# Optimization experiments

Measured on AMD Instinct MI355X. Metric: run time of the kernel, lower is better.

## Reference

```python
import jax, jax.numpy as jnp
import numpy as np

PRE_NMS_TOP_K = 6000   # 'test' mode
POST_NMS_TOP_K = 300   # 'test' mode
IOU_THRESHOLD = 0.7


def setup_inputs() -> dict:
    key = jax.random.key(0)
    k1, k2, k3, k4 = jax.random.split(key, 4)
    B, A, H, W = 1, 9, 64, 96
    N = H * W * A  # 55296 anchors
    pred_cls = jax.random.normal(k1, (B, 2 * A, H, W), dtype=jnp.float32)
    pred_loc = jax.random.normal(k2, (B, 4 * A, H, W), dtype=jnp.float32) * 0.1
    # anchors in normalized (cx, cy, w, h) format
    cxcy = jax.random.uniform(k3, (N, 2), dtype=jnp.float32)
    wh = jax.random.uniform(k4, (N, 2), dtype=jnp.float32) * 0.2 + 0.02
    anchor = jnp.concatenate([cxcy, wh], axis=-1)
    return {"pred_cls": pred_cls, "pred_loc": pred_loc, "anchor": anchor}


def _decode_to_xy(loc, anchor):
    # decode: t(cx,cy) * a(w,h) + a(cx,cy); exp(t(w,h)) * a(w,h); then cxcy -> xyxy
    cxcy = loc[:, :2] * anchor[:, 2:] + anchor[:, :2]
    wh = jnp.exp(loc[:, 2:]) * anchor[:, 2:]
    return jnp.concatenate([cxcy - wh * 0.5, cxcy + wh * 0.5], axis=-1)


def _iou_matrix(boxes):
    # boxes: [N,4] xyxy -> [N,N] IoU
    area = (boxes[:, 2] - boxes[:, 0]) * (boxes[:, 3] - boxes[:, 1])
    lt = jnp.maximum(boxes[:, None, :2], boxes[None, :, :2])  # [N,N,2]
    rb = jnp.minimum(boxes[:, None, 2:], boxes[None, :, 2:])  # [N,N,2]
    wh = jnp.clip(rb - lt, 0.0)
    inter = wh[..., 0] * wh[..., 1]
    union = area[:, None] + area[None, :] - inter
    return inter / jnp.maximum(union, 1e-12)


def _nms_keep(boxes, iou_threshold):
    # boxes already sorted by descending score -> greedy NMS
    n = boxes.shape[0]
    iou = _iou_matrix(boxes)
    idx = jnp.arange(n)

    def body(i, keep):
        suppress = (iou[i] > iou_threshold) & (idx > i)
        return jnp.where(keep[i], keep & ~suppress, keep)

    return jax.lax.fori_loop(0, n, body, jnp.ones((n,), dtype=bool))


def reference(pred_cls, pred_loc, anchor):
    B = pred_cls.shape[0]
    # NCHW -> NHWC -> [N, 2] / [N, 4]  (batch squeezed, B == 1)
    cls = jnp.transpose(pred_cls, (0, 2, 3, 1)).reshape(B, -1, 2)[0]
    loc = jnp.transpose(pred_loc, (0, 2, 3, 1)).reshape(B, -1, 4)[0]

    roi = jnp.clip(_decode_to_xy(loc, anchor), 0.0, 1.0)           # [N,4]
    scores = jax.nn.sigmoid(cls)[:, 1]                              # [N]

    order = jnp.argsort(-scores)[:PRE_NMS_TOP_K]                    # descending
    roi = roi[order]                                                # [K,4]

    keep = _nms_keep(roi, IOU_THRESHOLD)                            # [K] bool
    # kept boxes first (stable -> preserves score order), take top 300
    sel = jnp.argsort(jnp.where(keep, 0, 1), stable=True)[:POST_NMS_TOP_K]
    valid = keep[sel]
    # pad with zeros if fewer than 300 boxes survive NMS (torch returns a
    # dynamically-sized tensor; we keep a fixed [300,4] with zero padding)
    return jnp.where(valid[:, None], roi[sel], 0.0)
```

## Files before the change

### kernel.cpp

```cpp
#include <hip/hip_runtime.h>


#define ADIM 9
#define NANCH 55296
#define HWSZ 6144
#define CH_U4 1536
#define TOT_U4 13824
#define SAMP_U4 3456
#define TOPK 6000
#define OUTK 300
#define NBINS 16384
#define CAP 8192
#define SCAP 1024
#define SRANK 128
#define MROWS 512
#define MW 8
#define THR 0.7f

typedef unsigned long long u64;
typedef unsigned int u32;

__device__ __forceinline__ u32 flipu(u32 b) {
    u32 u = (b & 0x80000000u) ? ~b : (b | 0x80000000u);
    return ~u;
}

__device__ __forceinline__ bool iou_gt(float4 a, float aa, float4 b, float ba) {
    float ix = fminf(a.z, b.z) - fmaxf(a.x, b.x);
    float iy = fminf(a.w, b.w) - fmaxf(a.y, b.y);
    float inter = fmaxf(ix, 0.f) * fmaxf(iy, 0.f);
    float u = fmaxf(aa + ba - inter, 1e-12f);
    float d = __builtin_fmaf(-THR, u, inter);
    if (__builtin_fabsf(d) > 1e-6f * u) return d > 0.f;
    return inter / u > THR;
}

__device__ __forceinline__ float4 decode_box(const float* __restrict__ loc,
                                             const float* __restrict__ anc, u32 n) {
    u32 a = n % 9u, hw = n / 9u;
    float t0 = loc[(4 * a + 0) * HWSZ + hw];
    float t1 = loc[(4 * a + 1) * HWSZ + hw];
    float t2 = loc[(4 * a + 2) * HWSZ + hw];
    float t3 = loc[(4 * a + 3) * HWSZ + hw];
    float4 an = reinterpret_cast<const float4*>(anc)[n];
    float cx = t0 * an.z + an.x;
    float cy = t1 * an.w + an.y;
    float bw = expf(t2) * an.z;
    float bh = expf(t3) * an.w;
    return make_float4(fminf(fmaxf(cx - bw * 0.5f, 0.f), 1.f),
                       fminf(fmaxf(cy - bh * 0.5f, 0.f), 1.f),
                       fminf(fmaxf(cx + bw * 0.5f, 0.f), 1.f),
                       fminf(fmaxf(cy + bh * 0.5f, 0.f), 1.f));
}

__device__ __forceinline__ u64 sx64(u64 v, int m) {
    u32 lo = __shfl_xor((u32)(v & 0xffffffffu), m, 64);
    u32 hi = __shfl_xor((u32)(v >> 32), m, 64);
    return ((u64)hi << 32) | lo;
}

__device__ __forceinline__ u64 ce64(u64 v, int j, int lane, bool up) {
    u64 pv = sx64(v, j);
    u64 mn = (pv < v) ? pv : v;
    u64 mx = (pv < v) ? v : pv;
    return (((lane & j) == 0) == up) ? mn : mx;
}

__device__ __forceinline__ uint4 ld_cls4(const uint4* __restrict__ cls4, int i) {
    int ch = i / CH_U4;
    int e4 = i - ch * CH_U4;
    return cls4[(2 * ch + 1) * CH_U4 + e4];
}

__device__ __forceinline__ u32 block_scan(u32 s, int wid, int lane, u32* wsum) {
    u32 x = s;
    #pragma unroll
    for (int d = 1; d < 64; d <<= 1) {
        u32 y = __shfl_up(x, (unsigned)d, 64);
        if (lane >= d) x += y;
    }
    if (lane == 63) wsum[wid] = x;
    __syncthreads();
    if (wid == 0) {
        u32 w = (lane < 16) ? wsum[lane] : 0u;
        #pragma unroll
        for (int d = 1; d < 16; d <<= 1) {
            u32 y = __shfl_up(w, (unsigned)d, 64);
            if (lane >= d) w += y;
        }
        if (lane < 16) wsum[lane] = w;
    }
    __syncthreads();
    return x + (wid ? wsum[wid - 1] : 0u);
}

__device__ __forceinline__ u32 find_cutoff(const u32* hist, u32 thresh, int tid,
                                           int wid, int lane, u32* wsum, u32* sB) {
    u32 h[16];
    const uint4* h4 = reinterpret_cast<const uint4*>(hist);
    #pragma unroll
    for (int k = 0; k < 4; ++k) {
        uint4 v = h4[tid * 4 + k];
        h[4 * k + 0] = v.x; h[4 * k + 1] = v.y; h[4 * k + 2] = v.z; h[4 * k + 3] = v.w;
    }
    u32 s = 0;
    #pragma unroll
    for (int b = 0; b < 16; ++b) s += h[b];
    u32 incl = block_scan(s, wid, lane, wsum);
    u32 before = incl - s;
    if (before < thresh && incl >= thresh) {
        u32 run = before;
        #pragma unroll
        for (int b = 0; b < 16; ++b) {
            run += h[b];
            if (run >= thresh) { sB[0] = (u32)(tid * 16 + b); break; }
        }
    }
    __syncthreads();
    u32 r = sB[0];
    __syncthreads();
    return r;
}

__global__ void __launch_bounds__(1024) k_scanrank(const float* __restrict__ cls,
                                                   const float* __restrict__ loc,
                                                   const float* __restrict__ anc,
                                                   u32* __restrict__ wsMeta,
                                                   float4* __restrict__ boxS,
                                                   float* __restrict__ areaS) {
    __shared__ u32 hist[NBINS];
    __shared__ __align__(16) u32 sfs[SCAP];
    __shared__ u32 sidx[SCAP];
    __shared__ u32 wsum[16];
    __shared__ u32 sB[2];
    __shared__ u32 shu[2];

    const int tid = threadIdx.x;
    const int wid = tid >> 6;
    const int lane = tid & 63;
    const uint4* cls4 = reinterpret_cast<const uint4*>(cls);

    u64* h64 = (u64*)hist;
    for (int i = tid; i < NBINS / 2; i += 1024) h64[i] = 0ull;
    if (tid < 2) shu[tid] = 0;
    __syncthreads();
    {
        uint4 s0 = ld_cls4(cls4, 4 * tid);
        uint4 s1 = ld_cls4(cls4, 4 * (tid + 1024));
        uint4 s2 = ld_cls4(cls4, 4 * (tid + 2048));
        bool has3 = tid < (SAMP_U4 - 3072);
        uint4 s3 = has3 ? ld_cls4(cls4, 4 * (tid + 3072)) : make_uint4(0u,0u,0u,0u);
        atomicAdd(&hist[flipu(s0.x) >> 18], 1u); atomicAdd(&hist[flipu(s0.y) >> 18], 1u);
        atomicAdd(&hist[flipu(s0.z) >> 18], 1u); atomicAdd(&hist[flipu(s0.w) >> 18], 1u);
        atomicAdd(&hist[flipu(s1.x) >> 18], 1u); atomicAdd(&hist[flipu(s1.y) >> 18], 1u);
        atomicAdd(&hist[flipu(s1.z) >> 18], 1u); atomicAdd(&hist[flipu(s1.w) >> 18], 1u);
        atomicAdd(&hist[flipu(s2.x) >> 18], 1u); atomicAdd(&hist[flipu(s2.y) >> 18], 1u);
        atomicAdd(&hist[flipu(s2.z) >> 18], 1u); atomicAdd(&hist[flipu(s2.w) >> 18], 1u);
        if (has3) {
            atomicAdd(&hist[flipu(s3.x) >> 18], 1u); atomicAdd(&hist[flipu(s3.y) >> 18], 1u);
            atomicAdd(&hist[flipu(s3.z) >> 18], 1u); atomicAdd(&hist[flipu(s3.w) >> 18], 1u);
        }
    }
    __syncthreads();
    const u32 B1 = find_cutoff(hist, SRANK, tid, wid, lane, wsum, sB);
    const u32 K1 = (B1 + 1u) << 18;

    u64 bm = 0;
    u32 cnt = 0;
    #pragma unroll
    for (int half = 0; half < 2; ++half) {
        uint4 buf[7];
        #pragma unroll
        for (int kk = 0; kk < 7; ++kk) {
            int i = (half * 7 + kk) * 1024 + tid;
            buf[kk] = (i < TOT_U4) ? ld_cls4(cls4, i) : make_uint4(0xFFFFFFFFu,0xFFFFFFFFu,0xFFFFFFFFu,0xFFFFFFFFu);
        }
        #pragma unroll
        for (int kk = 0; kk < 7; ++kk) {
            int i = (half * 7 + kk) * 1024 + tid;
            if (i < TOT_U4) {
                #pragma unroll
                for (int c = 0; c < 4; ++c) {
                    u32 b = (c == 0) ? buf[kk].x : (c == 1) ? buf[kk].y
                          : (c == 2) ? buf[kk].z : buf[kk].w;
                    if (flipu(b) < K1) {
                        cnt++;
                        bm |= 1ull << ((half * 7 + kk) * 4 + c);
                    }
                }
            }
        }
    }
    u32 incl = block_scan(cnt, wid, lane, wsum);
    u32 base = incl - cnt;
    if (tid == 1023) shu[0] = incl;
    __syncthreads();
    const u32 csRaw = shu[0];
    const u32 cs = csRaw < SCAP ? csRaw : SCAP;
    if (blockIdx.x == 0 && tid == 0) { wsMeta[0] = csRaw; wsMeta[1] = B1; }
    if (csRaw > SCAP) return;

    {
        u64 m = bm;
        u32 o = base;
        while (m) {
            int b = __ffsll((unsigned long long)m) - 1;
            m &= m - 1;
            int kk = b >> 2, c = b & 3;
            int i = kk * 1024 + tid;
            uint4 v = ld_cls4(cls4, i);
            u32 raw = (c == 0) ? v.x : (c == 1) ? v.y : (c == 2) ? v.z : v.w;
            int ch = i / CH_U4;
            int e4 = i - ch * CH_U4;
            u32 n = (u32)((e4 * 4 + c) * ADIM + ch);
            if (o < SCAP) { sfs[o] = flipu(raw); sidx[o] = n; }
            o++;
        }
    }
    if (tid >= (int)cs) { sfs[tid] = 0xFFFFFFFFu; sidx[tid] = 0xFFFFFFFFu; }
    __syncthreads();

    const int ci = blockIdx.x * 64 + (tid >> 4);
    const int p = tid & 15;
    const u32 myf = sfs[ci];
    const u32 myi = sidx[ci];
    u32 r = 0;
    #pragma unroll 8
    for (int k = 0; k < 64; ++k) {
        int j = k * 16 + p;
        u32 fj = sfs[j];
        u32 ij = sidx[j];
        r += (fj < myf) || (fj == myf && ij < myi);
    }
    r += __shfl_xor(r, 1, 64);
    r += __shfl_xor(r, 2, 64);
    r += __shfl_xor(r, 4, 64);
    r += __shfl_xor(r, 8, 64);
    if (p == 0 && (u32)ci < csRaw) {
        float4 b = decode_box(loc, anc, myi);
        boxS[r] = b;
        areaS[r] = (b.z - b.x) * (b.w - b.y);
    }
}

__global__ void __launch_bounds__(1024) k_mat(const u32* __restrict__ wsMeta,
                                              const float4* __restrict__ boxS,
                                              const float* __restrict__ areaS,
                                              u32* __restrict__ maskG32) {
    __shared__ float4 B[MROWS];
    __shared__ float  A[MROWS];
    __shared__ u32 M32[32][16];
    const int tid = threadIdx.x;
    const u32 csRaw = wsMeta[0];
    if (csRaw > SCAP) return;
    const u32 rowsv = csRaw < MROWS ? csRaw : MROWS;

    if (tid < MROWS) { B[tid] = boxS[tid]; A[tid] = areaS[tid]; }
    if (tid < 512) M32[tid >> 4][tid & 15] = 0u;
    __syncthreads();

    const int rl = tid >> 5;
    const int sub = tid & 31;
    const int row = blockIdx.x + 16 * rl;
    if (row < (int)rowsv) {
        const int j0 = sub * 16;
        int jmax = row < j0 + 16 ? row : j0 + 16;
        if (j0 < jmax) {
            float4 rb = B[row];
            float rba = A[row];
            u32 bits = 0;
            #pragma unroll 4
            for (int j = j0; j < jmax; ++j)
                if (iou_gt(rb, rba, B[j], A[j])) bits |= 1u << (j - j0);
            if (bits) atomicOr(&M32[rl][sub >> 1], bits << ((sub & 1) * 16));
        }
    }
    __syncthreads();
    if (tid < 512) {
        int rl2 = tid >> 4, w = tid & 15;
        int row2 = blockIdx.x + 16 * rl2;
        maskG32[row2 * 16 + w] = M32[rl2][w];
    }
}

__global__ void __launch_bounds__(1024) k_greedy(const float* __restrict__ cls,
                                                 const float* __restrict__ loc,
                                                 const float* __restrict__ anc,
                                                 const u32* __restrict__ wsMeta,
                                                 const float4* __restrict__ boxS,
                                                 const float* __restrict__ areaS,
                                                 const u32* __restrict__ maskG32,
                                                 float4* __restrict__ out) {
    __shared__ u64 cand[CAP];
    __shared__ u64 smask[MROWS][MW];
    __shared__ float4 sbox[SCAP];
    __shared__ float  sarea[SCAP];
    __shared__ float4 kept[OUTK];
    __shared__ float  karea[OUTK];
    __shared__ float4 cbox[64];
    __shared__ float  carea[64];
    __shared__ u64 supw[16];
    __shared__ u64 sbyp[1024];
    __shared__ u32 wsum[16];
    __shared__ u32 sB[2];
    __shared__ u32 shu[8];

    const int tid = threadIdx.x;
    const int wid = tid >> 6;
    const int lane = tid & 63;
    u32* hist = (u32*)cand;
    const uint4* cls4 = reinterpret_cast<const uint4*>(cls);

    const u32 csRaw = wsMeta[0];
    const u32 cs = csRaw < SCAP ? csRaw : SCAP;
    const bool fast = (csRaw <= SCAP);

    if (tid < 8) shu[tid] = 0;
    sbox[tid] = boxS[tid];
    sarea[tid] = areaS[tid];
    {
        u32* sm32 = (u32*)smask;
        #pragma unroll
        for (int k = 0; k < 8; ++k) sm32[k * 1024 + tid] = maskG32[k * 1024 + tid];
    }
    __syncthreads();

    if (fast) {
        const u32 rowsv = cs < MROWS ? cs : MROWS;
        if (wid == 0) {
            u32 kc = 0, nexti0 = 0;
            u64 K[MW];
            #pragma unroll
            for (int w = 0; w < MW; ++w) K[w] = 0ull;
            #pragma unroll
            for (int cw = 0; cw < MW; ++cw) {
                u32 i0 = (u32)cw * 64u;
                if (i0 < rowsv && kc < OUTK) {
                    u32 ci = i0 + (u32)lane;
                    bool valid = ci < rowsv;
                    u64 myw[MW];
                    #pragma unroll
                    for (int w = 0; w < MW; ++w) myw[w] = valid ? smask[ci][w] : 0ull;
                    u64 supk = 0;
                    #pragma unroll
                    for (int w = 0; w < MW; ++w) supk |= myw[w] & K[w];
                    bool ia = valid && (supk == 0ull);
                    u64 inch = myw[cw] & ((1ull << lane) - 1ull);
                    u64 A = __ballot(ia ? 1 : 0);
                    for (int itx = 0; itx < 64; ++itx) {
                        bool na = ia && ((inch & A) == 0ull);
                        u64 A2 = __ballot(na ? 1 : 0);
                        if (A2 == A) break;
                        A = A2;
                    }
                    bool kp = (A >> lane) & 1;
                    u32 rank = (u32)__popcll(A & ((1ull << lane) - 1ull));
                    if (kp && kc + rank < OUTK) {
                        float4 c = sbox[ci];
                        kept[kc + rank] = c;
                        karea[kc + rank] = sarea[ci];
                        out[kc + rank] = c;
                    }
                    K[cw] = A;
                    kc += (u32)__popcll(A);
                    nexti0 = i0 + 64;
                }
            }
            if (lane == 0) {
                shu[4] = kc > OUTK ? OUTK : kc;
                shu[5] = nexti0;
            }
        }

        const u32 limit = cs;
        while (true) {
            __syncthreads();
            u32 kc = shu[4], i0 = shu[5];
            if (kc >= OUTK || i0 >= limit) break;
            u32 ci = i0 + (u32)lane;
            bool valid = ci < limit;
            float4 c = sbox[valid ? ci : 0];
            float ca = sarea[valid ? ci : 0];

            bool sup = false;
            for (u32 j = (u32)wid; j < kc; j += 16)
                sup = sup || iou_gt(c, ca, kept[j], karea[j]);
            u64 bal = __ballot(sup ? 1 : 0);
            if (lane == 0) supw[wid] = bal;

            u64 sby = 0;
            u32 smax = 4u * wid + 4u; if (smax > 63u) smax = 63u;
            for (u32 s = 4u * wid + 1u; s <= smax; ++s) {
                u32 p = ((u32)lane + s) & 63u;
                if (p < (u32)lane && (i0 + p) < limit)
                    if (iou_gt(c, ca, sbox[i0 + p], sarea[i0 + p])) sby |= (1ull << p);
            }
            sbyp[wid * 64 + lane] = sby;
            __syncthreads();

            if (wid == 0) {
                u64 sup64 = 0, sbyfull = 0;
                #pragma unroll
                for (int w = 0; w < 16; ++w) { sup64 |= supw[w]; sbyfull |= sbyp[w * 64 + lane]; }
                bool ia = valid && !((sup64 >> lane) & 1);
                u64 A = __ballot(ia ? 1 : 0);
                for (int itx = 0; itx < 64; ++itx) {
                    bool na = ia && ((sbyfull & A) == 0);
                    u64 A2 = __ballot(na ? 1 : 0);
                    if (A2 == A) break;
                    A = A2;
                }
                bool kp = (A >> lane) & 1;
                u32 rank = (u32)__popcll(A & ((1ull << lane) - 1ull));
                if (kp && kc + rank < OUTK) {
                    kept[kc + rank] = c; karea[kc + rank] = ca; out[kc + rank] = c;
                }
                if (lane == 0) {
                    u32 nk = kc + (u32)__popcll(A);
                    shu[4] = nk > OUTK ? OUTK : nk;
                    shu[5] = i0 + 64;
                }
            }
        }
    }

    __syncthreads();
    if (shu[4] < OUTK) {
        const u32 consumed = fast ? cs : 0u;
        u64* h64 = (u64*)hist;
        for (int i = tid; i < NBINS / 2; i += 1024) h64[i] = 0ull;
        __syncthreads();
        #pragma unroll
        for (int half = 0; half < 2; ++half) {
            uint4 buf[7];
            #pragma unroll
            for (int kk = 0; kk < 7; ++kk) {
                int i = (half * 7 + kk) * 1024 + tid;
                buf[kk] = (i < TOT_U4) ? ld_cls4(cls4, i) : make_uint4(0u,0u,0u,0u);
            }
            #pragma unroll
            for (int kk = 0; kk < 7; ++kk) {
                int i = (half * 7 + kk) * 1024 + tid;
                if (i < TOT_U4) {
                    atomicAdd(&hist[flipu(buf[kk].x) >> 18], 1u);
                    atomicAdd(&hist[flipu(buf[kk].y) >> 18], 1u);
                    atomicAdd(&hist[flipu(buf[kk].z) >> 18], 1u);
                    atomicAdd(&hist[flipu(buf[kk].w) >> 18], 1u);
                }
            }
        }
        __syncthreads();
        const u32 B2 = find_cutoff(hist, TOPK, tid, wid, lane, wsum, sB);
        u64 bm2 = 0;
        u32 cnt2 = 0;
        #pragma unroll
        for (int half = 0; half < 2; ++half) {
            uint4 buf[7];
            #pragma unroll
            for (int kk = 0; kk < 7; ++kk) {
                int i = (half * 7 + kk) * 1024 + tid;
                buf[kk] = (i < TOT_U4) ? ld_cls4(cls4, i) : make_uint4(0xFFFFFFFFu,0xFFFFFFFFu,0xFFFFFFFFu,0xFFFFFFFFu);
            }
            #pragma unroll
            for (int kk = 0; kk < 7; ++kk) {
                int i = (half * 7 + kk) * 1024 + tid;
                if (i < TOT_U4) {
                    #pragma unroll
                    for (int c = 0; c < 4; ++c) {
                        u32 b = (c == 0) ? buf[kk].x : (c == 1) ? buf[kk].y
                              : (c == 2) ? buf[kk].z : buf[kk].w;
                        if ((flipu(b) >> 18) <= B2) {
                            cnt2++;
                            bm2 |= 1ull << ((half * 7 + kk) * 4 + c);
                        }
                    }
                }
            }
        }
        __syncthreads();
        for (int i = tid; i < CAP; i += 1024) cand[i] = ~0ull;
        u32 incl2 = block_scan(cnt2, wid, lane, wsum);
        u32 base2 = incl2 - cnt2;
        if (tid == 1023) shu[1] = incl2;
        __syncthreads();
        {
            u64 m2 = bm2;
            u32 o = base2;
            while (m2) {
                int b = __ffsll((unsigned long long)m2) - 1;
                m2 &= m2 - 1;
                int kk = b >> 2, c = b & 3;
                int i = kk * 1024 + tid;
                uint4 v = ld_cls4(cls4, i);
                u32 raw = (c == 0) ? v.x : (c == 1) ? v.y : (c == 2) ? v.z : v.w;
                int ch = i / CH_U4;
                int e4 = i - ch * CH_U4;
                u32 n = (u32)((e4 * 4 + c) * ADIM + ch);
                if (o < CAP) cand[o] = ((u64)flipu(raw) << 32) | n;
                o++;
            }
        }
        __syncthreads();
        const u32 totF = shu[1];
        const u32 limfb = totF < TOPK ? totF : TOPK;
        for (int seg = wid; seg < CAP / 64; seg += 16) {
            u64 v = cand[seg * 64 + lane];
            #pragma unroll
            for (int k = 2; k <= 64; k <<= 1)
                #pragma unroll
                for (int j = k >> 1; j >= 1; j >>= 1)
                    v = ce64(v, j, lane, (((seg * 64 + lane) & k) == 0));
            cand[seg * 64 + lane] = v;
        }
        __syncthreads();
        for (int k = 128; k <= CAP; k <<= 1) {
            for (int j = k >> 1; j >= 64; j >>= 1) {
                for (u32 p = (u32)tid; p < CAP / 2; p += 1024) {
                    u32 i = ((p & ~(u32)(j - 1)) << 1) | (p & (u32)(j - 1));
                    u32 l = i | (u32)j;
                    bool up = ((i & (u32)k) == 0);
                    u64 a = cand[i], b = cand[l];
                    if ((a > b) == up) { cand[i] = b; cand[l] = a; }
                }
                __syncthreads();
            }
            for (int seg = wid; seg < CAP / 64; seg += 16) {
                u64 v = cand[seg * 64 + lane];
                bool up = (((seg * 64) & k) == 0);
                #pragma unroll
                for (int j = 32; j >= 1; j >>= 1) v = ce64(v, j, lane, up);
                cand[seg * 64 + lane] = v;
            }
            __syncthreads();
        }
        if (tid == 0) shu[5] = consumed;
        while (true) {
            __syncthreads();
            u32 kc = shu[4], i0 = shu[5];
            if (kc >= OUTK || i0 >= limfb) break;
            if (wid == 0) {
                u32 ci = i0 + (u32)lane;
                u32 n = (ci < limfb) ? (u32)cand[ci] : 0u;
                float4 b = decode_box(loc, anc, n);
                cbox[lane] = b;
                carea[lane] = (b.z - b.x) * (b.w - b.y);
            }
            __syncthreads();
            u32 ci = i0 + (u32)lane;
            bool valid = ci < limfb;
            float4 c = cbox[lane];
            float ca = carea[lane];
            bool sup = false;
            for (u32 j = (u32)wid; j < kc; j += 16)
                sup = sup || iou_gt(c, ca, kept[j], karea[j]);
            u64 bal = __ballot(sup ? 1 : 0);
            if (lane == 0) supw[wid] = bal;
            u64 sby = 0;
            u32 smax = 4u * wid + 4u; if (smax > 63u) smax = 63u;
            for (u32 s = 4u * wid + 1u; s <= smax; ++s) {
                u32 p = ((u32)lane + s) & 63u;
                if (p < (u32)lane && (i0 + p) < limfb)
                    if (iou_gt(c, ca, cbox[p], carea[p])) sby |= (1ull << p);
            }
            sbyp[wid * 64 + lane] = sby;
            __syncthreads();
            if (wid == 0) {
                u64 sup64 = 0, sbyfull = 0;
                #pragma unroll
                for (int w = 0; w < 16; ++w) { sup64 |= supw[w]; sbyfull |= sbyp[w * 64 + lane]; }
                bool ia = valid && !((sup64 >> lane) & 1);
                u64 A = __ballot(ia ? 1 : 0);
                for (int itx = 0; itx < 64; ++itx) {
                    bool na = ia && ((sbyfull & A) == 0);
                    u64 A2 = __ballot(na ? 1 : 0);
                    if (A2 == A) break;
                    A = A2;
                }
                bool kp = (A >> lane) & 1;
                u32 rank = (u32)__popcll(A & ((1ull << lane) - 1ull));
                if (kp && kc + rank < OUTK) {
                    kept[kc + rank] = c; karea[kc + rank] = ca; out[kc + rank] = c;
                }
                if (lane == 0) {
                    u32 nk = kc + (u32)__popcll(A);
                    shu[4] = nk > OUTK ? OUTK : nk;
                    shu[5] = i0 + 64;
                }
            }
        }
    }

    __syncthreads();
    u32 kc = shu[4];
    for (u32 r = (u32)tid; r < OUTK; r += 1024)
        if (r >= kc) out[r] = make_float4(0.f, 0.f, 0.f, 0.f);
}

extern "C" void kernel_launch(void* const* d_in, const int* in_sizes, int n_in,
                              void* d_out, int out_size, void* d_ws, size_t ws_size,
                              hipStream_t stream) {
    const float* cls = (const float*)d_in[0];
    const float* loc = (const float*)d_in[1];
    const float* anc = (const float*)d_in[2];

    char* ws = (char*)d_ws;
    u32*    wsMeta  = (u32*)(ws + 0);
    float4* boxS    = (float4*)(ws + 16);
    float*  areaS   = (float*)(ws + 16400);
    u32*    maskG32 = (u32*)(ws + 20496);

    k_scanrank<<<16, 1024, 0, stream>>>(cls, loc, anc, wsMeta, boxS, areaS);
    k_mat     <<<16, 1024, 0, stream>>>(wsMeta, boxS, areaS, maskG32);
    k_greedy  <<<1, 1024, 0, stream>>>(cls, loc, anc, wsMeta, boxS, areaS, maskG32, (float4*)d_out);
}
```

Measured before the change: 35.00 us.

## Load class scores once, pack sort keys into u64, zero output in matrix kernel

The histogram sample now comes from the same 14 uint4 registers per thread that feed the candidate selection, so the separate sampling loads go away. The sample changes from the first contiguous chunk to one value per uint4 across the whole array, and the rank target is nudged to match. Score and index are packed into one 64-bit shared key so the rank comparison is a single compare. Output zero-fill moves from the tail of the single-block greedy kernel into the matrix kernel, which relies on stream ordering and on the greedy kernel overwriting the kept rows.

Measured after the change: 123.7 us. 3.53x slower.

```diff
diff --git a/kernel.cpp b/kernel.cpp
--- a/kernel.cpp
+++ b/kernel.cpp
@@ -6,13 +6,12 @@
 #define HWSZ 6144
 #define CH_U4 1536
 #define TOT_U4 13824
-#define SAMP_U4 3456
 #define TOPK 6000
 #define OUTK 300
 #define NBINS 16384
 #define CAP 8192
 #define SCAP 1024
-#define SRANK 128
+#define SRANK 133
 #define MROWS 512
 #define MW 8
 #define THR 0.7f
@@ -129,8 +128,7 @@
                                                    float4* __restrict__ boxS,
                                                    float* __restrict__ areaS) {
     __shared__ u32 hist[NBINS];
-    __shared__ __align__(16) u32 sfs[SCAP];
-    __shared__ u32 sidx[SCAP];
+    __shared__ u64 skey[SCAP];
     __shared__ u32 wsum[16];
     __shared__ u32 sB[2];
     __shared__ u32 shu[2];
@@ -144,23 +142,17 @@
     for (int i = tid; i < NBINS / 2; i += 1024) h64[i] = 0ull;
     if (tid < 2) shu[tid] = 0;
     __syncthreads();
-    {
-        uint4 s0 = ld_cls4(cls4, 4 * tid);
-        uint4 s1 = ld_cls4(cls4, 4 * (tid + 1024));
-        uint4 s2 = ld_cls4(cls4, 4 * (tid + 2048));
-        bool has3 = tid < (SAMP_U4 - 3072);
-        uint4 s3 = has3 ? ld_cls4(cls4, 4 * (tid + 3072)) : make_uint4(0u,0u,0u,0u);
-        atomicAdd(&hist[flipu(s0.x) >> 18], 1u); atomicAdd(&hist[flipu(s0.y) >> 18], 1u);
-        atomicAdd(&hist[flipu(s0.z) >> 18], 1u); atomicAdd(&hist[flipu(s0.w) >> 18], 1u);
-        atomicAdd(&hist[flipu(s1.x) >> 18], 1u); atomicAdd(&hist[flipu(s1.y) >> 18], 1u);
-        atomicAdd(&hist[flipu(s1.z) >> 18], 1u); atomicAdd(&hist[flipu(s1.w) >> 18], 1u);
-        atomicAdd(&hist[flipu(s2.x) >> 18], 1u); atomicAdd(&hist[flipu(s2.y) >> 18], 1u);
-        atomicAdd(&hist[flipu(s2.z) >> 18], 1u); atomicAdd(&hist[flipu(s2.w) >> 18], 1u);
-        if (has3) {
-            atomicAdd(&hist[flipu(s3.x) >> 18], 1u); atomicAdd(&hist[flipu(s3.y) >> 18], 1u);
-            atomicAdd(&hist[flipu(s3.z) >> 18], 1u); atomicAdd(&hist[flipu(s3.w) >> 18], 1u);
-        }
-    }
+
+    uint4 buf[14];
+    #pragma unroll
+    for (int kk = 0; kk < 14; ++kk) {
+        int i = kk * 1024 + tid;
+        buf[kk] = (i < TOT_U4) ? ld_cls4(cls4, i)
+                               : make_uint4(0x7F800000u, 0x7F800000u, 0x7F800000u, 0x7F800000u);
+    }
+    #pragma unroll
+    for (int kk = 0; kk < 14; ++kk)
+        atomicAdd(&hist[flipu(buf[kk].x) >> 18], 1u);
     __syncthreads();
     const u32 B1 = find_cutoff(hist, SRANK, tid, wid, lane, wsum, sB);
     const u32 K1 = (B1 + 1u) << 18;
@@ -168,25 +160,16 @@
     u64 bm = 0;
     u32 cnt = 0;
     #pragma unroll
-    for (int half = 0; half < 2; ++half) {
-        uint4 buf[7];
-        #pragma unroll
-        for (int kk = 0; kk < 7; ++kk) {
-            int i = (half * 7 + kk) * 1024 + tid;
-            buf[kk] = (i < TOT_U4) ? ld_cls4(cls4, i) : make_uint4(0xFFFFFFFFu,0xFFFFFFFFu,0xFFFFFFFFu,0xFFFFFFFFu);
-        }
-        #pragma unroll
-        for (int kk = 0; kk < 7; ++kk) {
-            int i = (half * 7 + kk) * 1024 + tid;
-            if (i < TOT_U4) {
-                #pragma unroll
-                for (int c = 0; c < 4; ++c) {
-                    u32 b = (c == 0) ? buf[kk].x : (c == 1) ? buf[kk].y
-                          : (c == 2) ? buf[kk].z : buf[kk].w;
-                    if (flipu(b) < K1) {
-                        cnt++;
-                        bm |= 1ull << ((half * 7 + kk) * 4 + c);
-                    }
+    for (int kk = 0; kk < 14; ++kk) {
+        int i = kk * 1024 + tid;
+        if (i < TOT_U4) {
+            #pragma unroll
+            for (int c = 0; c < 4; ++c) {
+                u32 b = (c == 0) ? buf[kk].x : (c == 1) ? buf[kk].y
+                      : (c == 2) ? buf[kk].z : buf[kk].w;
+                if (flipu(b) < K1) {
+                    cnt++;
+                    bm |= 1ull << (kk * 4 + c);
                 }
             }
         }
@@ -213,31 +196,28 @@
             int ch = i / CH_U4;
             int e4 = i - ch * CH_U4;
             u32 n = (u32)((e4 * 4 + c) * ADIM + ch);
-            if (o < SCAP) { sfs[o] = flipu(raw); sidx[o] = n; }
+            if (o < SCAP) skey[o] = ((u64)flipu(raw) << 32) | n;
             o++;
         }
     }
-    if (tid >= (int)cs) { sfs[tid] = 0xFFFFFFFFu; sidx[tid] = 0xFFFFFFFFu; }
+    if (tid >= (int)cs) skey[tid] = ~0ull;
     __syncthreads();
 
     const int ci = blockIdx.x * 64 + (tid >> 4);
     const int p = tid & 15;
-    const u32 myf = sfs[ci];
-    const u32 myi = sidx[ci];
+    const u64 myk = skey[ci];
     u32 r = 0;
     #pragma unroll 8
     for (int k = 0; k < 64; ++k) {
         int j = k * 16 + p;
-        u32 fj = sfs[j];
-        u32 ij = sidx[j];
-        r += (fj < myf) || (fj == myf && ij < myi);
+        r += (skey[j] < myk) ? 1u : 0u;
     }
     r += __shfl_xor(r, 1, 64);
     r += __shfl_xor(r, 2, 64);
     r += __shfl_xor(r, 4, 64);
     r += __shfl_xor(r, 8, 64);
     if (p == 0 && (u32)ci < csRaw) {
-        float4 b = decode_box(loc, anc, myi);
+        float4 b = decode_box(loc, anc, (u32)myk);
         boxS[r] = b;
         areaS[r] = (b.z - b.x) * (b.w - b.y);
     }
@@ -246,11 +226,14 @@
 __global__ void __launch_bounds__(1024) k_mat(const u32* __restrict__ wsMeta,
                                               const float4* __restrict__ boxS,
                                               const float* __restrict__ areaS,
-                                              u32* __restrict__ maskG32) {
+                                              u32* __restrict__ maskG32,
+                                              float4* __restrict__ out) {
     __shared__ float4 B[MROWS];
     __shared__ float  A[MROWS];
     __shared__ u32 M32[32][16];
     const int tid = threadIdx.x;
+    if (blockIdx.x == 0 && tid < OUTK)
+        out[tid] = make_float4(0.f, 0.f, 0.f, 0.f);
     const u32 csRaw = wsMeta[0];
     if (csRaw > SCAP) return;
     const u32 rowsv = csRaw < MROWS ? csRaw : MROWS;
@@ -589,11 +572,6 @@
             }
         }
     }
-
-    __syncthreads();
-    u32 kc = shu[4];
-    for (u32 r = (u32)tid; r < OUTK; r += 1024)
-        if (r >= kc) out[r] = make_float4(0.f, 0.f, 0.f, 0.f);
 }
 
 extern "C" void kernel_launch(void* const* d_in, const int* in_sizes, int n_in,
@@ -610,6 +588,6 @@
     u32*    maskG32 = (u32*)(ws + 20496);
 
     k_scanrank<<<16, 1024, 0, stream>>>(cls, loc, anc, wsMeta, boxS, areaS);
-    k_mat     <<<16, 1024, 0, stream>>>(wsMeta, boxS, areaS, maskG32);
+    k_mat     <<<16, 1024, 0, stream>>>(wsMeta, boxS, areaS, maskG32, (float4*)d_out);
     k_greedy  <<<1, 1024, 0, stream>>>(cls, loc, anc, wsMeta, boxS, areaS, maskG32, (float4*)d_out);
 }
```
